# Performance work log

Hardware: AMD Instinct MI355X
Metric: run time of the kernel (lower is better)

The kernel has to match this reference:

```python
import jax, jax.numpy as jnp
import numpy as np

NUM_CLASSES = 10

def setup_inputs() -> dict:
    key = jax.random.key(0)
    k1, k2, k3 = jax.random.split(key, 3)
    X = jax.random.normal(k1, (1024, 128), dtype=jnp.float32)
    X_train = jax.random.normal(k2, (100000, 128), dtype=jnp.float32)
    y_train = jax.random.randint(k3, (100000,), 0, NUM_CLASSES, dtype=jnp.int64)
    return {"X": X, "X_train": X_train, "y_train": y_train, "k": 5}


def reference(X, X_train, y_train, k):
    test_sq = jnp.sum(X * X, axis=1, keepdims=True)            # [T, 1]
    train_sq = jnp.sum(X_train * X_train, axis=1)[None, :]     # [1, N]
    cross = X @ X_train.T                                      # [T, N]
    dists = jnp.sqrt(jnp.maximum(test_sq + train_sq - 2.0 * cross, 0.0))
    # top-k nearest: smallest distances == largest negated distances
    _, idx = jax.lax.top_k(-dists, k)                          # [T, k]
    labels = y_train[idx]                                      # [T, k]
    # majority vote; argmax returns the smallest label on ties,
    # matching most_frq_smaller semantics
    counts = jnp.sum(jax.nn.one_hot(labels, NUM_CLASSES, dtype=jnp.int32), axis=1)  # [T, C]
    y_pred = jnp.argmax(counts, axis=1).astype(jnp.float32)    # torch.zeros default float
    return y_pred
```

## Files before the change

kernel.cpp:

```cpp
#include <hip/hip_runtime.h>
#include <cfloat>
#include <cstdint>


#define NTRAIN 100000
#define D 128
#define T 1024
#define TB 128
#define NT 32
#define KNN 5
#define NUM_CLASSES 10
#define NCH 160
#define CHUNK 640
#define NSUB 128
#define SCHUNK 64
#define NTILE_TOT 3125
#define TILE_HALVES 8192
#define SBS 132

typedef _Float16 half8 __attribute__((ext_vector_type(8)));
typedef float f32x16 __attribute__((ext_vector_type(16)));

#define MFMA(a, b, c) __builtin_amdgcn_mfma_f32_32x32x16_f16((a), (b), (c), 0, 0, 0)

struct Cand { float s; int j; };

__device__ __forceinline__ bool better(float s, int j, const Cand& c) {
    return (s > c.s) || (s == c.s && j < c.j);
}

__device__ __forceinline__ void ins5(Cand t5[KNN], float s, int j) {
    if (!better(s, j, t5[4])) return;
    if (better(s, j, t5[0]))      { t5[4]=t5[3]; t5[3]=t5[2]; t5[2]=t5[1]; t5[1]=t5[0]; t5[0]={s,j}; }
    else if (better(s, j, t5[1])) { t5[4]=t5[3]; t5[3]=t5[2]; t5[2]=t5[1]; t5[1]={s,j}; }
    else if (better(s, j, t5[2])) { t5[4]=t5[3]; t5[3]=t5[2]; t5[2]={s,j}; }
    else if (better(s, j, t5[3])) { t5[4]=t5[3]; t5[3]={s,j}; }
    else                          { t5[4]={s,j}; }
}

__device__ __forceinline__ void ins5f(float b[KNN], float s) {
    if (!(s > b[4])) return;
    if (s > b[0])      { b[4]=b[3]; b[3]=b[2]; b[2]=b[1]; b[1]=b[0]; b[0]=s; }
    else if (s > b[1]) { b[4]=b[3]; b[3]=b[2]; b[2]=b[1]; b[1]=s; }
    else if (s > b[2]) { b[4]=b[3]; b[3]=b[2]; b[2]=s; }
    else if (s > b[3]) { b[4]=b[3]; b[3]=s; }
    else               { b[4]=s; }
}

__device__ __forceinline__ void gload_lds16(const void* g, void* l) {
    __builtin_amdgcn_global_load_lds(
        (const __attribute__((address_space(1))) uint32_t*)g,
        (__attribute__((address_space(3))) uint32_t*)l, 16, 0, 0);
}

__global__ __launch_bounds__(256)
void knn_norms(const float* __restrict__ XT, uint32_t* __restrict__ nrmp) {
    const int j = blockIdx.x * 256 + threadIdx.x;
    if (j >= NTRAIN) return;
    const float4* row = (const float4*)&XT[(size_t)j * D];
    float p[32];
#pragma unroll
    for (int c = 0; c < 32; ++c) {
        float4 v = row[c];
        p[c] = v.x * v.x + v.y * v.y + v.z * v.z + v.w * v.w;
    }
#pragma unroll
    for (int s = 1; s < 32; s <<= 1)
#pragma unroll
        for (int i = 0; i < 32; i += 2 * s) p[i] += p[i + s];
    const float m = -0.5f * p[0];
    const _Float16 mh = (_Float16)m;
    const _Float16 ml = (_Float16)(m - (float)mh);
    union { _Float16 h[2]; uint32_t u; } cv;
    cv.h[0] = mh; cv.h[1] = ml;
    nrmp[j] = cv.u;
}

__global__ __launch_bounds__(256)
void knn_pack(const float* __restrict__ XT, _Float16* __restrict__ XTs,
              uint32_t* __restrict__ nrmp) {
    __shared__ __align__(16) float sb[32 * SBS];
    const int tid  = threadIdx.x;
    const int tile = blockIdx.x;
    const float4* src = (const float4*)&XT[(size_t)tile * 32 * D];
#pragma unroll
    for (int p = 0; p < 4; ++p) {
        const int i4  = p * 256 + tid;
        const int row = i4 >> 5;
        const int c4  = i4 & 31;
        *(float4*)&sb[row * SBS + c4 * 4] = src[i4];
    }
    __syncthreads();

    {
        const int ks = tid >> 5, kh = (tid >> 4) & 1, rp = (tid & 15) * 2;
        const int c0 = ks * 16 + kh * 8;
        _Float16* outp = &XTs[(size_t)tile * TILE_HALVES + tid * 16];
#pragma unroll
        for (int rr = 0; rr < 2; ++rr) {
            const float* s = &sb[(rp + rr) * SBS + c0];
            half8 hv, lv;
#pragma unroll
            for (int e = 0; e < 8; ++e) {
                float v = s[e];
                _Float16 hh = (_Float16)v;
                hv[e] = hh; lv[e] = (_Float16)(v - (float)hh);
            }
            *(half8*)&outp[rr * 8]        = hv;
            *(half8*)&outp[4096 + rr * 8] = lv;
        }
    }
    {
        const int row = tid >> 3, seg = tid & 7;
        const float4* rp4 = (const float4*)&sb[row * SBS];
        float q[4];
#pragma unroll
        for (int c = 0; c < 4; ++c) {
            float4 v = rp4[seg * 4 + c];
            q[c] = v.x * v.x + v.y * v.y + v.z * v.z + v.w * v.w;
        }
        float part = (q[0] + q[1]) + (q[2] + q[3]);
        part += __shfl_xor(part, 1);
        part += __shfl_xor(part, 2);
        part += __shfl_xor(part, 4);
        if (seg == 0) {
            const float m = -0.5f * part;
            const _Float16 mh = (_Float16)m;
            const _Float16 ml = (_Float16)(m - (float)mh);
            union { _Float16 h[2]; uint32_t u; } cv;
            cv.h[0] = mh; cv.h[1] = ml;
            nrmp[tile * 32 + row] = cv.u;
        }
    }
}

template <bool SPLIT, bool THRESH>
__global__ __launch_bounds__(256, 4)
void knn_mfma(const float* __restrict__ X, const float* __restrict__ XT,
              const _Float16* __restrict__ XTs, const uint32_t* __restrict__ nrmp,
              Cand* __restrict__ part, int nch, int chunk,
              const float* __restrict__ thrb, float* __restrict__ thrc5) {
    __shared__ __align__(16) _Float16 lds[2][TILE_HALVES];

    const int tid  = threadIdx.x;
    const int lane = tid & 63;
    const int wv   = tid >> 6;

    const int L   = blockIdx.x;
    const int xcd = L & 7;
    const int s_  = L >> 3;
    const int bx  = s_ & 7;
    const int bc  = (s_ & ~7) | xcd;
    if (bc >= nch) return;

    half8 Bh[8], Bl[8];
    {
        const int trow = bx * TB + wv * 32 + (lane & 31);
        const float* xp = &X[(size_t)trow * D + (lane >> 5) * 8];
#pragma unroll
        for (int ks = 0; ks < 8; ++ks) {
            float4 v0 = *(const float4*)&xp[ks * 16];
            float4 v1 = *(const float4*)&xp[ks * 16 + 4];
            float a[8] = {v0.x, v0.y, v0.z, v0.w, v1.x, v1.y, v1.z, v1.w};
#pragma unroll
            for (int e = 0; e < 8; ++e) {
                _Float16 hh = (_Float16)a[e];
                Bh[ks][e] = hh;
                Bl[ks][e] = (_Float16)(a[e] - (float)hh);
            }
        }
    }
    half8 B8;
#pragma unroll
    for (int e = 0; e < 8; ++e) B8[e] = (_Float16)0.0f;
    if (lane < 32) B8[0] = (_Float16)1.0f;

    f32x16 kZero;
#pragma unroll
    for (int e = 0; e < 16; ++e) kZero[e] = 0.f;

    const int srow = tid & 31;
    const int ksp  = tid >> 5;
    float a16[16];

    auto issue_stage_split = [&](int buf, int tile) {
        int tl = tile; if (tl > NTILE_TOT - 1) tl = NTILE_TOT - 1;
        const _Float16* g = &XTs[(size_t)tl * TILE_HALVES + wv * 512 + lane * 8];
        _Float16* l = &lds[buf][wv * 512];
#pragma unroll
        for (int p = 0; p < 4; ++p)
            gload_lds16(g + p * 2048, l + p * 2048);
    };
    auto issue_loads = [&](int jb) {
        int j = jb + srow;
        if (j > NTRAIN - 1) j = NTRAIN - 1;
        const float4* p = (const float4*)&XT[(size_t)j * D + ksp * 16];
        float4 v0 = p[0], v1 = p[1], v2 = p[2], v3 = p[3];
        a16[0]=v0.x; a16[1]=v0.y; a16[2]=v0.z; a16[3]=v0.w;
        a16[4]=v1.x; a16[5]=v1.y; a16[6]=v1.z; a16[7]=v1.w;
        a16[8]=v2.x; a16[9]=v2.y; a16[10]=v2.z; a16[11]=v2.w;
        a16[12]=v3.x; a16[13]=v3.y; a16[14]=v3.z; a16[15]=v3.w;
    };
    auto write_stage = [&](int buf) {
        half8 hv0, lv0, hv1, lv1;
#pragma unroll
        for (int e = 0; e < 8; ++e) {
            _Float16 hh = (_Float16)a16[e];
            hv0[e] = hh; lv0[e] = (_Float16)(a16[e] - (float)hh);
        }
#pragma unroll
        for (int e = 0; e < 8; ++e) {
            _Float16 hh = (_Float16)a16[8 + e];
            hv1[e] = hh; lv1[e] = (_Float16)(a16[8 + e] - (float)hh);
        }
        _Float16* base = &lds[buf][ksp * 512 + srow * 8];
        *(half8*)(base)              = hv0;
        *(half8*)(base + 256)        = hv1;
        *(half8*)(base + 4096)       = lv0;
        *(half8*)(base + 4096 + 256) = lv1;
    };

    float s0 = -FLT_MAX;
    if (!THRESH && thrb != nullptr) {
        const int col = bx * TB + wv * 32 + (lane & 31);
        s0 = thrb[col];
    }
    Cand top5[KNN];
#pragma unroll
    for (int e = 0; e < KNN; ++e) top5[e] = {s0, 0x7fffffff};

    const int jc0 = bc * chunk;
    const int ntiles = chunk >> 5;
    const int tile0 = jc0 >> 5;

    if (SPLIT) {
        issue_stage_split(0, tile0);
    } else {
        issue_loads(jc0);
        write_stage(0);
    }
    __syncthreads();

    for (int t = 0; t < ntiles; ++t) {
        const int jb = jc0 + t * NT;
        if (!SPLIT && jb >= NTRAIN) break;
        const int buf = t & 1;
        const bool more = (t + 1 < ntiles);

        if (SPLIT) {
            if (more) issue_stage_split(buf ^ 1, tile0 + t + 1);
        } else {
            if (more) issue_loads(jb + NT);
        }

        int nj = jb + (lane & 31);
        if (nj > NTRAIN - 1) nj = NTRAIN - 1;
        uint32_t nv = nrmp[nj];
        if (lane >= 32) nv = 0;

        const _Float16* rbase = &lds[buf][lane * 8];
        __builtin_amdgcn_s_setprio(1);
        f32x16 acc;
        {
            half8 ah = *(const half8*)(rbase);
            half8 al = *(const half8*)(rbase + 4096);
            acc = MFMA(ah, Bh[0], kZero);
            acc = MFMA(ah, Bl[0], acc);
            acc = MFMA(al, Bh[0], acc);
        }
#pragma unroll
        for (int ks = 1; ks < 8; ++ks) {
            half8 ah = *(const half8*)(rbase + ks * 512);
            half8 al = *(const half8*)(rbase + 4096 + ks * 512);
            acc = MFMA(ah, Bh[ks], acc);
            acc = MFMA(ah, Bl[ks], acc);
            acc = MFMA(al, Bh[ks], acc);
        }
        {
            union { uint32_t u; _Float16 h[2]; } cv; cv.u = nv;
            half8 augh, augl;
#pragma unroll
            for (int e = 0; e < 8; ++e) { augh[e] = (_Float16)0.0f; augl[e] = (_Float16)0.0f; }
            augh[0] = cv.h[0];
            augl[0] = cv.h[1];
            acc = MFMA(augh, B8, acc);
            acc = MFMA(augl, B8, acc);
        }
        __builtin_amdgcn_s_setprio(0);

        if (!SPLIT && more) write_stage(buf ^ 1);

        __syncthreads();

        const int rb = 4 * (lane >> 5);
#pragma unroll
        for (int reg = 0; reg < 16; ++reg) {
            const float s = acc[reg];
            if (s >= top5[4].s) {
                const int j = jb + (reg & 3) + 8 * (reg >> 2) + rb;
                if (j < NTRAIN) ins5(top5, s, j);
            }
        }
    }

    {
        float os[KNN]; int oj[KNN];
#pragma unroll
        for (int e = 0; e < KNN; ++e) {
            os[e] = __shfl_xor(top5[e].s, 32);
            oj[e] = __shfl_xor(top5[e].j, 32);
        }
#pragma unroll
        for (int e = 0; e < KNN; ++e) ins5(top5, os[e], oj[e]);
        if (lane < 32) {
            const int test = bx * TB + wv * 32 + lane;
            if (THRESH) {
                float* pp = &thrc5[((size_t)test * NSUB + bc) * KNN];
#pragma unroll
                for (int e = 0; e < KNN; ++e) pp[e] = top5[e].s;
            } else {
                Cand* pp = &part[((size_t)test * nch + bc) * KNN];
#pragma unroll
                for (int e = 0; e < KNN; ++e) pp[e] = top5[e];
            }
        }
    }
}

__global__ __launch_bounds__(256)
void knn_thrmerge(const float* __restrict__ thrc5, float* __restrict__ thr) {
    const int tid  = threadIdx.x;
    const int lane = tid & 63;
    const int test = blockIdx.x * 4 + (tid >> 6);
    if (test >= T) return;

    float b[KNN];
#pragma unroll
    for (int e = 0; e < KNN; ++e) b[e] = -FLT_MAX;

    for (int c = lane; c < NSUB; c += 64) {
        const float* pp = &thrc5[((size_t)test * NSUB + c) * KNN];
#pragma unroll
        for (int e = 0; e < KNN; ++e) ins5f(b, pp[e]);
    }
#pragma unroll
    for (int off = 32; off >= 1; off >>= 1) {
        float os[KNN];
#pragma unroll
        for (int e = 0; e < KNN; ++e) os[e] = __shfl_xor(b[e], off);
#pragma unroll
        for (int e = 0; e < KNN; ++e) ins5f(b, os[e]);
    }
    if (lane == 0) thr[test] = b[4];
}

__global__ __launch_bounds__(256)
void knn_vote2(const Cand* __restrict__ part, const int* __restrict__ y,
               float* __restrict__ out, int nch) {
    const int tid  = threadIdx.x;
    const int lane = tid & 63;
    const int test = blockIdx.x * 4 + (tid >> 6);
    if (test >= T) return;

    Cand best[KNN];
#pragma unroll
    for (int e = 0; e < KNN; ++e) best[e] = {-FLT_MAX, 0x7fffffff};

    for (int c = lane; c < nch; c += 64) {
        const Cand* pp = &part[((size_t)test * nch + c) * KNN];
#pragma unroll
        for (int e = 0; e < KNN; ++e) {
            const Cand cc = pp[e];
            if ((unsigned)cc.j < (unsigned)NTRAIN) ins5(best, cc.s, cc.j);
        }
    }
#pragma unroll
    for (int off = 32; off >= 1; off >>= 1) {
        float os[KNN]; int oj[KNN];
#pragma unroll
        for (int e = 0; e < KNN; ++e) {
            os[e] = __shfl_xor(best[e].s, off);
            oj[e] = __shfl_xor(best[e].j, off);
        }
#pragma unroll
        for (int e = 0; e < KNN; ++e)
            if ((unsigned)oj[e] < (unsigned)NTRAIN) ins5(best, os[e], oj[e]);
    }
    if (lane == 0) {
        int lbl[KNN];
#pragma unroll
        for (int e = 0; e < KNN; ++e) lbl[e] = y[best[e].j];
        int bestc = 0, bestcnt = -1;
#pragma unroll
        for (int c = 0; c < NUM_CLASSES; ++c) {
            int cnt = 0;
#pragma unroll
            for (int e = 0; e < KNN; ++e) cnt += (lbl[e] == c) ? 1 : 0;
            if (cnt > bestcnt) { bestcnt = cnt; bestc = c; }
        }
        out[test] = (float)bestc;
    }
}

static inline int grid_for(int nch) {
    return 8 * (((nch + 7) / 8) * 8);
}

extern "C" void kernel_launch(void* const* d_in, const int* in_sizes, int n_in,
                              void* d_out, int out_size, void* d_ws, size_t ws_size,
                              hipStream_t stream) {
    const float* X  = (const float*)d_in[0];
    const float* XT = (const float*)d_in[1];
    const int*   y  = (const int*)d_in[2];

    const size_t xts_bytes  = (size_t)NTILE_TOT * TILE_HALVES * 2;
    const size_t nrm_bytes  = ((size_t)NTRAIN * 4 + 255) & ~(size_t)255;
    const size_t thr_bytes  = ((size_t)T * 4 + 255) & ~(size_t)255;
    const size_t per_chunk  = (size_t)T * KNN * sizeof(Cand);
    const size_t part_bytes = (size_t)NCH * per_chunk;

    const size_t need_full = xts_bytes + nrm_bytes + thr_bytes + part_bytes;
    const size_t need_noth = xts_bytes + nrm_bytes + part_bytes;

    if (ws_size >= need_full) {
        _Float16* XTs  = (_Float16*)d_ws;
        uint32_t* nrmp = (uint32_t*)((char*)d_ws + xts_bytes);
        float*    thr  = (float*)((char*)d_ws + xts_bytes + nrm_bytes);
        Cand*     part = (Cand*)((char*)d_ws + xts_bytes + nrm_bytes + thr_bytes);
        float*    thrc5 = (float*)part;
        knn_pack<<<NTILE_TOT, 256, 0, stream>>>(XT, XTs, nrmp);
        knn_mfma<true, true><<<grid_for(NSUB), 256, 0, stream>>>(
            X, XT, XTs, nrmp, nullptr, NSUB, SCHUNK, nullptr, thrc5);
        knn_thrmerge<<<T / 4, 256, 0, stream>>>(thrc5, thr);
        knn_mfma<true, false><<<grid_for(NCH), 256, 0, stream>>>(
            X, XT, XTs, nrmp, part, NCH, CHUNK, thr, nullptr);
        knn_vote2<<<T / 4, 256, 0, stream>>>(part, y, (float*)d_out, NCH);
    } else if (ws_size >= need_noth) {
        _Float16* XTs  = (_Float16*)d_ws;
        uint32_t* nrmp = (uint32_t*)((char*)d_ws + xts_bytes);
        Cand*     part = (Cand*)((char*)d_ws + xts_bytes + nrm_bytes);
        knn_pack<<<NTILE_TOT, 256, 0, stream>>>(XT, XTs, nrmp);
        knn_mfma<true, false><<<grid_for(NCH), 256, 0, stream>>>(
            X, XT, XTs, nrmp, part, NCH, CHUNK, nullptr, nullptr);
        knn_vote2<<<T / 4, 256, 0, stream>>>(part, y, (float*)d_out, NCH);
    } else {
        uint32_t* nrmp = (uint32_t*)d_ws;
        Cand*     part = (Cand*)((char*)d_ws + nrm_bytes);
        int fch = NCH;
        if (nrm_bytes + (size_t)fch * per_chunk > ws_size) {
            size_t avail = (ws_size > nrm_bytes) ? (ws_size - nrm_bytes) : 0;
            fch = (int)(avail / per_chunk);
            if (fch < 1) fch = 1;
        }
        const int chunk = (((NTRAIN + fch - 1) / fch) + (NT - 1)) & ~(NT - 1);
        knn_norms<<<(NTRAIN + 255) / 256, 256, 0, stream>>>(XT, nrmp);
        knn_mfma<false, false><<<grid_for(fch), 256, 0, stream>>>(
            X, XT, nullptr, nrmp, part, fch, chunk, nullptr, nullptr);
        knn_vote2<<<T / 4, 256, 0, stream>>>(part, y, (float*)d_out, fch);
    }
}
```

Baseline: 153.9 us.

## Load packed train tiles directly from global into registers, dropping LDS staging

The main distance kernel now reads packed fp16 hi/lo train tiles straight from global memory into MFMA operand registers instead of staging them through double-buffered LDS with per-tile barriers. Each wave works independently, so __syncthreads and LDS traffic disappear, and occupancy bounds drop to 3 blocks per SM. Chunking also changes from 160 chunks of 640 rows to 125 chunks of 800 rows. The risk is exposed global-load latency without explicit prefetch, plus each wave separately re-reading the same tile, which depends on L1/L2 hits.

```diff
diff --git a/kernel.cpp b/kernel.cpp
--- a/kernel.cpp
+++ b/kernel.cpp
@@ -10,8 +10,8 @@
 #define NT 32
 #define KNN 5
 #define NUM_CLASSES 10
-#define NCH 160
-#define CHUNK 640
+#define NCH 125
+#define CHUNK 800
 #define NSUB 128
 #define SCHUNK 64
 #define NTILE_TOT 3125
@@ -134,14 +134,12 @@
     }
 }
 
-template <bool SPLIT, bool THRESH>
-__global__ __launch_bounds__(256, 4)
-void knn_mfma(const float* __restrict__ X, const float* __restrict__ XT,
-              const _Float16* __restrict__ XTs, const uint32_t* __restrict__ nrmp,
-              Cand* __restrict__ part, int nch, int chunk,
-              const float* __restrict__ thrb, float* __restrict__ thrc5) {
-    __shared__ __align__(16) _Float16 lds[2][TILE_HALVES];
-
+template <bool THRESH>
+__global__ __launch_bounds__(256, 3)
+void knn_mfma_reg(const float* __restrict__ X, const _Float16* __restrict__ XTs,
+                  const uint32_t* __restrict__ nrmp, Cand* __restrict__ part,
+                  int nch, int chunk, const float* __restrict__ thrb,
+                  float* __restrict__ thrc5) {
     const int tid  = threadIdx.x;
     const int lane = tid & 63;
     const int wv   = tid >> 6;
@@ -153,9 +151,11 @@
     const int bc  = (s_ & ~7) | xcd;
     if (bc >= nch) return;
 
+    const int tg = bx * 4 + wv;
+
     half8 Bh[8], Bl[8];
     {
-        const int trow = bx * TB + wv * 32 + (lane & 31);
+        const int trow = tg * 32 + (lane & 31);
         const float* xp = &X[(size_t)trow * D + (lane >> 5) * 8];
 #pragma unroll
         for (int ks = 0; ks < 8; ++ks) {
@@ -179,18 +179,134 @@
 #pragma unroll
     for (int e = 0; e < 16; ++e) kZero[e] = 0.f;
 
+    float s0 = -FLT_MAX;
+    if (!THRESH && thrb != nullptr) s0 = thrb[tg * 32 + (lane & 31)];
+    Cand top5[KNN];
+#pragma unroll
+    for (int e = 0; e < KNN; ++e) top5[e] = {s0, 0x7fffffff};
+
+    const int jc0 = bc * chunk;
+    const int ntiles = chunk >> 5;
+    const int tile0 = jc0 >> 5;
+
+    const _Float16* gbase = &XTs[(size_t)tile0 * TILE_HALVES + lane * 8];
+
+    for (int t = 0; t < ntiles; ++t) {
+        const int jb = jc0 + t * NT;
+        const _Float16* gt = gbase + (size_t)t * TILE_HALVES;
+
+        int nj = jb + (lane & 31);
+        if (nj > NTRAIN - 1) nj = NTRAIN - 1;
+        uint32_t nv = nrmp[nj];
+        if (lane >= 32) nv = 0;
+
+        __builtin_amdgcn_s_setprio(1);
+        f32x16 acc;
+        {
+            half8 ah = *(const half8*)(gt);
+            half8 al = *(const half8*)(gt + 4096);
+            acc = MFMA(ah, Bh[0], kZero);
+            acc = MFMA(ah, Bl[0], acc);
+            acc = MFMA(al, Bh[0], acc);
+        }
+#pragma unroll
+        for (int ks = 1; ks < 8; ++ks) {
+            half8 ah = *(const half8*)(gt + ks * 512);
+            half8 al = *(const half8*)(gt + 4096 + ks * 512);
+            acc = MFMA(ah, Bh[ks], acc);
+            acc = MFMA(ah, Bl[ks], acc);
+            acc = MFMA(al, Bh[ks], acc);
+        }
+        {
+            union { uint32_t u; _Float16 h[2]; } cv; cv.u = nv;
+            half8 augh, augl;
+#pragma unroll
+            for (int e = 0; e < 8; ++e) { augh[e] = (_Float16)0.0f; augl[e] = (_Float16)0.0f; }
+            augh[0] = cv.h[0];
+            augl[0] = cv.h[1];
+            acc = MFMA(augh, B8, acc);
+            acc = MFMA(augl, B8, acc);
+        }
+        __builtin_amdgcn_s_setprio(0);
+
+        const int rb = 4 * (lane >> 5);
+#pragma unroll
+        for (int reg = 0; reg < 16; ++reg) {
+            const float s = acc[reg];
+            if (s >= top5[4].s) {
+                const int j = jb + (reg & 3) + 8 * (reg >> 2) + rb;
+                if (j < NTRAIN) ins5(top5, s, j);
+            }
+        }
+    }
+
+    {
+        float os[KNN]; int oj[KNN];
+#pragma unroll
+        for (int e = 0; e < KNN; ++e) {
+            os[e] = __shfl_xor(top5[e].s, 32);
+            oj[e] = __shfl_xor(top5[e].j, 32);
+        }
+#pragma unroll
+        for (int e = 0; e < KNN; ++e) ins5(top5, os[e], oj[e]);
+        if (lane < 32) {
+            const int test = tg * 32 + lane;
+            if (THRESH) {
+                float* pp = &thrc5[((size_t)test * NSUB + bc) * KNN];
+#pragma unroll
+                for (int e = 0; e < KNN; ++e) pp[e] = top5[e].s;
+            } else {
+                Cand* pp = &part[((size_t)test * nch + bc) * KNN];
+#pragma unroll
+                for (int e = 0; e < KNN; ++e) pp[e] = top5[e];
+            }
+        }
+    }
+}
+
+__global__ __launch_bounds__(256, 4)
+void knn_mfma_legacy(const float* __restrict__ X, const float* __restrict__ XT,
+                     const uint32_t* __restrict__ nrmp, Cand* __restrict__ part,
+                     int nch, int chunk) {
+    __shared__ __align__(16) _Float16 lds[2][TILE_HALVES];
+    const int tid  = threadIdx.x;
+    const int lane = tid & 63;
+    const int wv   = tid >> 6;
+    const int L   = blockIdx.x;
+    const int xcd = L & 7;
+    const int s_  = L >> 3;
+    const int bx  = s_ & 7;
+    const int bc  = (s_ & ~7) | xcd;
+    if (bc >= nch) return;
+
+    half8 Bh[8], Bl[8];
+    {
+        const int trow = bx * TB + wv * 32 + (lane & 31);
+        const float* xp = &X[(size_t)trow * D + (lane >> 5) * 8];
+#pragma unroll
+        for (int ks = 0; ks < 8; ++ks) {
+            float4 v0 = *(const float4*)&xp[ks * 16];
+            float4 v1 = *(const float4*)&xp[ks * 16 + 4];
+            float a[8] = {v0.x, v0.y, v0.z, v0.w, v1.x, v1.y, v1.z, v1.w};
+#pragma unroll
+            for (int e = 0; e < 8; ++e) {
+                _Float16 hh = (_Float16)a[e];
+                Bh[ks][e] = hh;
+                Bl[ks][e] = (_Float16)(a[e] - (float)hh);
+            }
+        }
+    }
+    half8 B8;
+#pragma unroll
+    for (int e = 0; e < 8; ++e) B8[e] = (_Float16)0.0f;
+    if (lane < 32) B8[0] = (_Float16)1.0f;
+    f32x16 kZero;
+#pragma unroll
+    for (int e = 0; e < 16; ++e) kZero[e] = 0.f;
+
     const int srow = tid & 31;
     const int ksp  = tid >> 5;
     float a16[16];
-
-    auto issue_stage_split = [&](int buf, int tile) {
-        int tl = tile; if (tl > NTILE_TOT - 1) tl = NTILE_TOT - 1;
-        const _Float16* g = &XTs[(size_t)tl * TILE_HALVES + wv * 512 + lane * 8];
-        _Float16* l = &lds[buf][wv * 512];
-#pragma unroll
-        for (int p = 0; p < 4; ++p)
-            gload_lds16(g + p * 2048, l + p * 2048);
-    };
     auto issue_loads = [&](int jb) {
         int j = jb + srow;
         if (j > NTRAIN - 1) j = NTRAIN - 1;
@@ -220,38 +336,22 @@
         *(half8*)(base + 4096 + 256) = lv1;
     };
 
-    float s0 = -FLT_MAX;
-    if (!THRESH && thrb != nullptr) {
-        const int col = bx * TB + wv * 32 + (lane & 31);
-        s0 = thrb[col];
-    }
     Cand top5[KNN];
 #pragma unroll
-    for (int e = 0; e < KNN; ++e) top5[e] = {s0, 0x7fffffff};
+    for (int e = 0; e < KNN; ++e) top5[e] = {-FLT_MAX, 0x7fffffff};
 
     const int jc0 = bc * chunk;
     const int ntiles = chunk >> 5;
-    const int tile0 = jc0 >> 5;
-
-    if (SPLIT) {
-        issue_stage_split(0, tile0);
-    } else {
-        issue_loads(jc0);
-        write_stage(0);
-    }
+    issue_loads(jc0);
+    write_stage(0);
     __syncthreads();
 
     for (int t = 0; t < ntiles; ++t) {
         const int jb = jc0 + t * NT;
-        if (!SPLIT && jb >= NTRAIN) break;
+        if (jb >= NTRAIN) break;
         const int buf = t & 1;
         const bool more = (t + 1 < ntiles);
-
-        if (SPLIT) {
-            if (more) issue_stage_split(buf ^ 1, tile0 + t + 1);
-        } else {
-            if (more) issue_loads(jb + NT);
-        }
+        if (more) issue_loads(jb + NT);
 
         int nj = jb + (lane & 31);
         if (nj > NTRAIN - 1) nj = NTRAIN - 1;
@@ -259,7 +359,6 @@
         if (lane >= 32) nv = 0;
 
         const _Float16* rbase = &lds[buf][lane * 8];
-        __builtin_amdgcn_s_setprio(1);
         f32x16 acc;
         {
             half8 ah = *(const half8*)(rbase);
@@ -286,10 +385,7 @@
             acc = MFMA(augh, B8, acc);
             acc = MFMA(augl, B8, acc);
         }
-        __builtin_amdgcn_s_setprio(0);
-
-        if (!SPLIT && more) write_stage(buf ^ 1);
-
+        if (more) write_stage(buf ^ 1);
         __syncthreads();
 
         const int rb = 4 * (lane >> 5);
@@ -302,7 +398,6 @@
             }
         }
     }
-
     {
         float os[KNN]; int oj[KNN];
 #pragma unroll
@@ -314,15 +409,9 @@
         for (int e = 0; e < KNN; ++e) ins5(top5, os[e], oj[e]);
         if (lane < 32) {
             const int test = bx * TB + wv * 32 + lane;
-            if (THRESH) {
-                float* pp = &thrc5[((size_t)test * NSUB + bc) * KNN];
-#pragma unroll
-                for (int e = 0; e < KNN; ++e) pp[e] = top5[e].s;
-            } else {
-                Cand* pp = &part[((size_t)test * nch + bc) * KNN];
-#pragma unroll
-                for (int e = 0; e < KNN; ++e) pp[e] = top5[e];
-            }
+            Cand* pp = &part[((size_t)test * nch + bc) * KNN];
+#pragma unroll
+            for (int e = 0; e < KNN; ++e) pp[e] = top5[e];
         }
     }
 }
@@ -429,19 +518,19 @@
         Cand*     part = (Cand*)((char*)d_ws + xts_bytes + nrm_bytes + thr_bytes);
         float*    thrc5 = (float*)part;
         knn_pack<<<NTILE_TOT, 256, 0, stream>>>(XT, XTs, nrmp);
-        knn_mfma<true, true><<<grid_for(NSUB), 256, 0, stream>>>(
-            X, XT, XTs, nrmp, nullptr, NSUB, SCHUNK, nullptr, thrc5);
+        knn_mfma_reg<true><<<grid_for(NSUB), 256, 0, stream>>>(
+            X, XTs, nrmp, nullptr, NSUB, SCHUNK, nullptr, thrc5);
         knn_thrmerge<<<T / 4, 256, 0, stream>>>(thrc5, thr);
-        knn_mfma<true, false><<<grid_for(NCH), 256, 0, stream>>>(
-            X, XT, XTs, nrmp, part, NCH, CHUNK, thr, nullptr);
+        knn_mfma_reg<false><<<grid_for(NCH), 256, 0, stream>>>(
+            X, XTs, nrmp, part, NCH, CHUNK, thr, nullptr);
         knn_vote2<<<T / 4, 256, 0, stream>>>(part, y, (float*)d_out, NCH);
     } else if (ws_size >= need_noth) {
         _Float16* XTs  = (_Float16*)d_ws;
         uint32_t* nrmp = (uint32_t*)((char*)d_ws + xts_bytes);
         Cand*     part = (Cand*)((char*)d_ws + xts_bytes + nrm_bytes);
         knn_pack<<<NTILE_TOT, 256, 0, stream>>>(XT, XTs, nrmp);
-        knn_mfma<true, false><<<grid_for(NCH), 256, 0, stream>>>(
-            X, XT, XTs, nrmp, part, NCH, CHUNK, nullptr, nullptr);
+        knn_mfma_reg<false><<<grid_for(NCH), 256, 0, stream>>>(
+            X, XTs, nrmp, part, NCH, CHUNK, nullptr, nullptr);
         knn_vote2<<<T / 4, 256, 0, stream>>>(part, y, (float*)d_out, NCH);
     } else {
         uint32_t* nrmp = (uint32_t*)d_ws;
@@ -454,8 +543,8 @@
         }
         const int chunk = (((NTRAIN + fch - 1) / fch) + (NT - 1)) & ~(NT - 1);
         knn_norms<<<(NTRAIN + 255) / 256, 256, 0, stream>>>(XT, nrmp);
-        knn_mfma<false, false><<<grid_for(fch), 256, 0, stream>>>(
-            X, XT, nullptr, nrmp, part, fch, chunk, nullptr, nullptr);
+        knn_mfma_legacy<<<grid_for(fch), 256, 0, stream>>>(
+            X, XT, nrmp, part, fch, chunk);
         knn_vote2<<<T / 4, 256, 0, stream>>>(part, y, (float*)d_out, fch);
     }
 }
```

Result: slower. 168.2 us (+9.3%).

## Retune train chunking to 125x800, drop LDS staging in pack kernel, simplify split loop

Applied to the files above, without the earlier changes.

Changes the train-set partition from 160 chunks of 640 to 125 chunks of 800 so chunks align exactly with 32-row tiles, which lets the split path drop tile clamping and bounds checks. The pack kernel now reads global memory directly instead of staging each tile through shared memory, removing a sync and an LDS round trip. The split loop advances a precomputed global pointer rather than recomputing tile addresses each iteration. Fewer chunks means fewer blocks and longer per-block loops, which may affect occupancy and the later merge stage.

```diff
diff --git a/kernel.cpp b/kernel.cpp
--- a/kernel.cpp
+++ b/kernel.cpp
@@ -10,13 +10,12 @@
 #define NT 32
 #define KNN 5
 #define NUM_CLASSES 10
-#define NCH 160
-#define CHUNK 640
+#define NCH 125
+#define CHUNK 800
 #define NSUB 128
 #define SCHUNK 64
 #define NTILE_TOT 3125
 #define TILE_HALVES 8192
-#define SBS 132
 
 typedef _Float16 half8 __attribute__((ext_vector_type(8)));
 typedef float f32x16 __attribute__((ext_vector_type(16)));
@@ -79,18 +78,9 @@
 __global__ __launch_bounds__(256)
 void knn_pack(const float* __restrict__ XT, _Float16* __restrict__ XTs,
               uint32_t* __restrict__ nrmp) {
-    __shared__ __align__(16) float sb[32 * SBS];
     const int tid  = threadIdx.x;
     const int tile = blockIdx.x;
-    const float4* src = (const float4*)&XT[(size_t)tile * 32 * D];
-#pragma unroll
-    for (int p = 0; p < 4; ++p) {
-        const int i4  = p * 256 + tid;
-        const int row = i4 >> 5;
-        const int c4  = i4 & 31;
-        *(float4*)&sb[row * SBS + c4 * 4] = src[i4];
-    }
-    __syncthreads();
+    const float* base = &XT[(size_t)tile * 32 * D];
 
     {
         const int ks = tid >> 5, kh = (tid >> 4) & 1, rp = (tid & 15) * 2;
@@ -98,11 +88,14 @@
         _Float16* outp = &XTs[(size_t)tile * TILE_HALVES + tid * 16];
 #pragma unroll
         for (int rr = 0; rr < 2; ++rr) {
-            const float* s = &sb[(rp + rr) * SBS + c0];
+            const float* s = &base[(rp + rr) * D + c0];
+            float4 v0 = *(const float4*)&s[0];
+            float4 v1 = *(const float4*)&s[4];
+            float a[8] = {v0.x, v0.y, v0.z, v0.w, v1.x, v1.y, v1.z, v1.w};
             half8 hv, lv;
 #pragma unroll
             for (int e = 0; e < 8; ++e) {
-                float v = s[e];
+                float v = a[e];
                 _Float16 hh = (_Float16)v;
                 hv[e] = hh; lv[e] = (_Float16)(v - (float)hh);
             }
@@ -112,7 +105,7 @@
     }
     {
         const int row = tid >> 3, seg = tid & 7;
-        const float4* rp4 = (const float4*)&sb[row * SBS];
+        const float4* rp4 = (const float4*)&base[row * D];
         float q[4];
 #pragma unroll
         for (int c = 0; c < 4; ++c) {
@@ -183,10 +176,11 @@
     const int ksp  = tid >> 5;
     float a16[16];
 
-    auto issue_stage_split = [&](int buf, int tile) {
-        int tl = tile; if (tl > NTILE_TOT - 1) tl = NTILE_TOT - 1;
-        const _Float16* g = &XTs[(size_t)tl * TILE_HALVES + wv * 512 + lane * 8];
-        _Float16* l = &lds[buf][wv * 512];
+    _Float16* const l0 = &lds[0][wv * 512];
+    _Float16* const l1 = &lds[1][wv * 512];
+
+    auto issue_stage_split = [&](int buf, const _Float16* g) {
+        _Float16* l = buf ? l1 : l0;
 #pragma unroll
         for (int p = 0; p < 4; ++p)
             gload_lds16(g + p * 2048, l + p * 2048);
@@ -233,8 +227,10 @@
     const int ntiles = chunk >> 5;
     const int tile0 = jc0 >> 5;
 
+    const _Float16* gcur = &XTs[(size_t)tile0 * TILE_HALVES + wv * 512 + lane * 8];
+
     if (SPLIT) {
-        issue_stage_split(0, tile0);
+        issue_stage_split(0, gcur);
     } else {
         issue_loads(jc0);
         write_stage(0);
@@ -248,13 +244,14 @@
         const bool more = (t + 1 < ntiles);
 
         if (SPLIT) {
-            if (more) issue_stage_split(buf ^ 1, tile0 + t + 1);
+            gcur += TILE_HALVES;
+            if (more) issue_stage_split(buf ^ 1, gcur);
         } else {
             if (more) issue_loads(jb + NT);
         }
 
         int nj = jb + (lane & 31);
-        if (nj > NTRAIN - 1) nj = NTRAIN - 1;
+        if (!SPLIT && nj > NTRAIN - 1) nj = NTRAIN - 1;
         uint32_t nv = nrmp[nj];
         if (lane >= 32) nv = 0;
 
@@ -298,7 +295,7 @@
             const float s = acc[reg];
             if (s >= top5[4].s) {
                 const int j = jb + (reg & 3) + 8 * (reg >> 2) + rb;
-                if (j < NTRAIN) ins5(top5, s, j);
+                if (SPLIT || j < NTRAIN) ins5(top5, s, j);
             }
         }
     }
```

Result: faster. 148.8 us (median of 2 runs) (-3.3%).
